# Kernel optimization log

Measured on AMD Instinct MI355X. Metric: run time of the kernel, lower is better.

## Reference

```python
import jax, jax.numpy as jnp
import numpy as np

B, S, H, NH = 8, 2048, 128, 4
HS = H // NH
EPS = 1e-8


def setup_inputs() -> dict:
    key = jax.random.key(0)
    ks = jax.random.split(key, 20)
    sc = 1.0 / np.sqrt(H)
    d = {
        'item_embeds': jax.random.normal(ks[0], (B, S, H), jnp.float32),
        'behavior_embeds': jax.random.normal(ks[1], (B, S, H), jnp.float32),
        'attn_mask': jnp.zeros((B, 1, S, S), jnp.float32),
    }
    names = ['Wq', 'Wk', 'Wv', 'Wqb', 'Wkb', 'Wvb', 'Wf']
    for i, n in enumerate(names):
        d[n] = jax.random.normal(ks[2 + i], (H, H), jnp.float32) * sc
        d['b' + n[1:]] = jnp.zeros((H,), jnp.float32)
    d['ln_w'] = jnp.ones((H,), jnp.float32)
    d['ln_b'] = jnp.zeros((H,), jnp.float32)
    return d


def _split_heads(x):
    # [B,S,H] -> [B,NH,S,HS]
    return x.reshape(B, S, NH, HS).transpose(0, 2, 1, 3)


def _layer_norm(x, w, b):
    u = jnp.mean(x, -1, keepdims=True)
    s = jnp.mean((x - u) ** 2, -1, keepdims=True)
    return w * ((x - u) / jnp.sqrt(s + EPS)) + b


def reference(item_embeds, behavior_embeds, attn_mask,
              Wq, bq, Wk, bk, Wv, bv,
              Wqb, bqb, Wkb, bkb, Wvb, bvb,
              Wf, bf, ln_w, ln_b):
    Q = _split_heads(item_embeds @ Wq + bq)
    K = _split_heads(item_embeds @ Wk + bk)
    V = _split_heads(item_embeds @ Wv + bv)
    Qb = _split_heads(behavior_embeds @ Wqb + bqb)
    Kb = _split_heads(behavior_embeds @ Wkb + bkb)
    # V_behavior computed in the original forward but unused downstream
    _Vb = _split_heads(behavior_embeds @ Wvb + bvb)
    scores = (jnp.einsum('bhqd,bhkd->bhqk', Q, K)
              + jnp.einsum('bhqd,bhkd->bhqk', Qb, Kb)) / np.sqrt(HS)
    scores = scores + attn_mask
    probs = jax.nn.softmax(scores, axis=-1)
    attn_out = jnp.einsum('bhqk,bhkd->bhqd', probs, V)
    attn_out = attn_out.transpose(0, 2, 1, 3).reshape(B, S, H)
    out = attn_out @ Wf + bf
    return _layer_norm(out + item_embeds, ln_w, ln_b)
```

## Files before the change

kernel.cpp:

```cpp
#include <hip/hip_runtime.h>
#include <math.h>

typedef unsigned short ushort_t;
typedef __attribute__((ext_vector_type(8))) short bf16x8;
typedef __attribute__((ext_vector_type(4))) float f32x4;

namespace {
constexpr int B = 8, S = 2048, H = 128, NH = 4, HS = 32;
constexpr float EPS = 1e-8f;
constexpr float SCALE = 0.17677669529663687f;
constexpr float LOG2E = 1.4426950408889634f;
constexpr float SCALEL = SCALE * LOG2E;
constexpr int QT = 16, KT = 64;
constexpr int KS = 2;
constexpr int SKT = S / KS / KT;
constexpr int NE = B * S * H;
}

__device__ __forceinline__ ushort_t f2bf(float f) {
  unsigned u = __float_as_uint(f);
  unsigned r = (u + 0x7FFFu + ((u >> 16) & 1u)) >> 16;
  return (ushort_t)r;
}

__device__ __forceinline__ f32x4 mfma16(bf16x8 a, bf16x8 b, f32x4 c) {
  return __builtin_amdgcn_mfma_f32_16x16x32_bf16(a, b, c, 0, 0, 0);
}

__global__ __launch_bounds__(256) void mflag_kernel(
    const float* __restrict__ mask, unsigned* __restrict__ fm)
{
  const int qt = blockIdx.x;
  const int b  = blockIdx.y;
  const int z  = blockIdx.z;
  const int t = threadIdx.x;
  const int lt = t >> 6;
  const int lane = t & 63;
  const float* mp = mask + ((long)b * S + (long)qt * QT + (lane >> 4) * 4) * S
                  + z * 256 + lt * 64 + (lane & 15) * 4;
  float s = 0.f;
#pragma unroll
  for (int rr = 0; rr < 4; ++rr) {
    const float4 a = *(const float4*)&mp[(long)rr * S];
    s += fabsf(a.x) + fabsf(a.y) + fabsf(a.z) + fabsf(a.w);
  }
  s += __shfl_xor(s, 1);
  s += __shfl_xor(s, 2);
  s += __shfl_xor(s, 4);
  s += __shfl_xor(s, 8);
  s += __shfl_xor(s, 16);
  s += __shfl_xor(s, 32);
  if (lane == 0 && !(s == 0.f))
    atomicOr(&fm[b * (S / QT) + qt], 1u << (z * 4 + lt));
}

__global__ __launch_bounds__(256) void wcvt_kernel(
    const float* __restrict__ Wq, const float* __restrict__ Wk, const float* __restrict__ Wv,
    const float* __restrict__ Wqb, const float* __restrict__ Wkb, const float* __restrict__ Wf,
    ushort_t* __restrict__ Wt)
{
  const float* Ws[6] = {Wq, Wk, Wv, Wqb, Wkb, Wf};
  const float scl[6] = {SCALEL, 1.f, 1.f, SCALEL, 1.f, 1.f};
  const int m = blockIdx.y;
  const int kb = blockIdx.x;
  const float* W = Ws[m];
  const float sc = scl[m];
  __shared__ float T[32 * 132];
  const int t = threadIdx.x;
#pragma unroll
  for (int u = 0; u < 4; ++u) {
    const int idx = u * 256 + t;
    const int row = idx >> 5, c4 = idx & 31;
    const float4 v = *(const float4*)&W[(kb * 32 + row) * H + c4 * 4];
    *(float4*)&T[row * 132 + c4 * 4] = v;
  }
  __syncthreads();
#pragma unroll
  for (int u = 0; u < 16; ++u) {
    const int idx = u * 256 + t;
    const int n = idx >> 5, kk = idx & 31;
    Wt[m * (H * H) + n * H + kb * 32 + kk] = f2bf(T[kk * 132 + n] * sc);
  }
}

__global__ __launch_bounds__(256) void proj_kernel(
    const float* __restrict__ item, const float* __restrict__ beh,
    const ushort_t* __restrict__ Wt,
    const float* __restrict__ bq, const float* __restrict__ bk, const float* __restrict__ bv,
    const float* __restrict__ bqb, const float* __restrict__ bkb,
    ushort_t* __restrict__ Qo, ushort_t* __restrict__ Ko, ushort_t* __restrict__ Qbo,
    ushort_t* __restrict__ Kbo, ushort_t* __restrict__ Vto)
{
  __shared__ ushort_t Xi[16 * 136];
  __shared__ ushort_t Xb[16 * 136];
  __shared__ ushort_t Yb[5][16 * 136];
  const int t = threadIdx.x;
  const long r0 = (long)blockIdx.x * 16;
#pragma unroll
  for (int u = 0; u < 2; ++u) {
    const int idx = u * 256 + t;
    const int row = idx >> 5, c4 = idx & 31;
    const float4 vi = *(const float4*)&item[(r0 + row) * H + c4 * 4];
    const float4 vb = *(const float4*)&beh[(r0 + row) * H + c4 * 4];
    unsigned long long pi = (unsigned long long)f2bf(vi.x) | ((unsigned long long)f2bf(vi.y) << 16)
        | ((unsigned long long)f2bf(vi.z) << 32) | ((unsigned long long)f2bf(vi.w) << 48);
    unsigned long long pb = (unsigned long long)f2bf(vb.x) | ((unsigned long long)f2bf(vb.y) << 16)
        | ((unsigned long long)f2bf(vb.z) << 32) | ((unsigned long long)f2bf(vb.w) << 48);
    *(unsigned long long*)&Xi[row * 136 + c4 * 4] = pi;
    *(unsigned long long*)&Xb[row * 136 + c4 * 4] = pb;
  }
  __syncthreads();

  const int w = t >> 6, l = t & 63, l15 = l & 15, quad = l >> 4;
  const int bb = (int)(r0 >> 11);
  const int s0 = (int)(r0 & (S - 1));
  const float* bias[5] = {bq, bk, bv, bqb, bkb};
  const float bscale[5] = {SCALEL, 1.f, 1.f, SCALEL, 1.f};

  bf16x8 afi[4], afb[4];
#pragma unroll
  for (int ks = 0; ks < 4; ++ks) {
    afi[ks] = *(const bf16x8*)&Xi[l15 * 136 + ks * 32 + quad * 8];
    afb[ks] = *(const bf16x8*)&Xb[l15 * 136 + ks * 32 + quad * 8];
  }

#pragma unroll
  for (int p = 0; p < 5; ++p) {
    f32x4 acc[2];
#pragma unroll
    for (int nt = 0; nt < 2; ++nt) {
      const float bcol = bias[p][w * 32 + nt * 16 + l15] * bscale[p];
      acc[nt] = (f32x4){bcol, bcol, bcol, bcol};
    }
    const ushort_t* Wp = Wt + p * (H * H);
    const bf16x8* af = (p < 3) ? afi : afb;
#pragma unroll
    for (int ks = 0; ks < 4; ++ks) {
      bf16x8 bfr[2];
#pragma unroll
      for (int nt = 0; nt < 2; ++nt)
        bfr[nt] = *(const bf16x8*)&Wp[(w * 32 + nt * 16 + l15) * H + ks * 32 + quad * 8];
#pragma unroll
      for (int nt = 0; nt < 2; ++nt)
        acc[nt] = mfma16(af[ks], bfr[nt], acc[nt]);
    }
#pragma unroll
    for (int nt = 0; nt < 2; ++nt)
#pragma unroll
      for (int r = 0; r < 4; ++r)
        Yb[p][(quad * 4 + r) * 136 + w * 32 + nt * 16 + l15] = f2bf(acc[nt][r]);
  }
  __syncthreads();
  {
    const int row = t >> 4, cb = (t & 15) * 8;
    const int h = cb >> 5, dd = cb & 31;
    const long gidx = ((long)(bb * NH + h) * S + s0 + row) * HS + dd;
    ushort_t* dsts4[4] = {Qo, Ko, Qbo, Kbo};
    const int psrc[4] = {0, 1, 3, 4};
#pragma unroll
    for (int i = 0; i < 4; ++i)
      *(uint4*)&dsts4[i][gidx] = *(const uint4*)&Yb[psrc[i]][row * 136 + cb];
    const int d = t >> 1, sh = (t & 1) * 8;
    const int nt = (s0 >> 4) & 3;
    const long vbase = ((long)(bb * NH + (d >> 5)) * HS + (d & 31)) * S + (s0 & ~63) + nt;
#pragma unroll
    for (int i = 0; i < 8; ++i)
      Vto[vbase + (long)(sh + i) * 4] = Yb[2][(sh + i) * 136 + d];
  }
}

__global__ __launch_bounds__(256, 4) void attn_kernel(
    const ushort_t* __restrict__ Q, const ushort_t* __restrict__ K,
    const ushort_t* __restrict__ Qb, const ushort_t* __restrict__ Kb,
    const ushort_t* __restrict__ Vt, const float* __restrict__ mask,
    const unsigned* __restrict__ fmg,
    ushort_t* __restrict__ PO, float* __restrict__ lsumP)
{
  __shared__ ushort_t Pb[NH][16 * 72];
  const int t = threadIdx.x;
  const int w = t >> 6;
  const int l15 = t & 15, quad = (t & 63) >> 4;
  const int q0 = blockIdx.x * QT;
  const int b = blockIdx.y;
  const int kz = blockIdx.z;
  const int kbase = kz * (S / KS);
  const long hQ = (long)(b * NH + w) * S * HS;
  const long hV = (long)(b * NH + w) * HS * S;

  const bf16x8 qf  = *(const bf16x8*)&Q[hQ + (long)(q0 + l15) * HS + quad * 8];
  const bf16x8 qbf = *(const bf16x8*)&Qb[hQ + (long)(q0 + l15) * HS + quad * 8];

  const unsigned fm = fmg[b * (S / QT) + blockIdx.x];

  const float* mrow[4];
#pragma unroll
  for (int r = 0; r < 4; ++r)
    mrow[r] = mask + ((long)b * S + q0 + quad * 4 + r) * S + l15;

  float lsum[4] = {0.f, 0.f, 0.f, 0.f};
  f32x4 O[2];
#pragma unroll
  for (int dt = 0; dt < 2; ++dt) O[dt] = (f32x4){0.f, 0.f, 0.f, 0.f};
  ushort_t* Pw = Pb[w];

  for (int i = 0; i < SKT; ++i) {
    const int k0 = kbase + i * KT;
    bf16x8 kf[4], kbf[4], vf[2][2];
#pragma unroll
    for (int nt = 0; nt < 4; ++nt) {
      kf[nt]  = *(const bf16x8*)&K[hQ + (long)(k0 + nt * 16 + l15) * HS + quad * 8];
      kbf[nt] = *(const bf16x8*)&Kb[hQ + (long)(k0 + nt * 16 + l15) * HS + quad * 8];
    }
#pragma unroll
    for (int dt = 0; dt < 2; ++dt)
#pragma unroll
      for (int ks = 0; ks < 2; ++ks)
        vf[dt][ks] = *(const bf16x8*)&Vt[hV + (long)(dt * 16 + l15) * S + k0 + ks * 32 + quad * 8];
    f32x4 sc[4];
    if ((fm >> (kz * SKT + i)) & 1u) {
#pragma unroll
      for (int nt = 0; nt < 4; ++nt)
#pragma unroll
        for (int r = 0; r < 4; ++r)
          sc[nt][r] = mrow[r][k0 + nt * 16] * LOG2E;
    } else {
#pragma unroll
      for (int nt = 0; nt < 4; ++nt)
        sc[nt] = (f32x4){0.f, 0.f, 0.f, 0.f};
    }
#pragma unroll
    for (int nt = 0; nt < 4; ++nt) {
      sc[nt] = mfma16(qbf, kbf[nt], sc[nt]);
      sc[nt] = mfma16(qf, kf[nt], sc[nt]);
    }
#pragma unroll
    for (int nt = 0; nt < 4; ++nt)
#pragma unroll
      for (int r = 0; r < 4; ++r)
        sc[nt][r] = __builtin_amdgcn_exp2f(sc[nt][r]);
#pragma unroll
    for (int r = 0; r < 4; ++r)
      lsum[r] += sc[0][r] + sc[1][r] + sc[2][r] + sc[3][r];
#pragma unroll
    for (int r = 0; r < 4; ++r) {
      const unsigned long long pk =
            (unsigned long long)(__float_as_uint(sc[0][r]) >> 16)
          | ((unsigned long long)(__float_as_uint(sc[1][r]) >> 16) << 16)
          | ((unsigned long long)(__float_as_uint(sc[2][r]) >> 16) << 32)
          | ((unsigned long long)(__float_as_uint(sc[3][r]) >> 16) << 48);
      *(unsigned long long*)&Pw[(quad * 4 + r) * 72 + l15 * 4] = pk;
    }
    bf16x8 pf[2];
#pragma unroll
    for (int ks = 0; ks < 2; ++ks)
      pf[ks] = *(const bf16x8*)&Pw[l15 * 72 + ks * 32 + quad * 8];
#pragma unroll
    for (int dt = 0; dt < 2; ++dt)
#pragma unroll
      for (int ks = 0; ks < 2; ++ks)
        O[dt] = mfma16(pf[ks], vf[dt][ks], O[dt]);
  }
#pragma unroll
  for (int r = 0; r < 4; ++r) {
    float s = lsum[r];
    s += __shfl_xor(s, 1);
    s += __shfl_xor(s, 2);
    s += __shfl_xor(s, 4);
    s += __shfl_xor(s, 8);
    lsum[r] = s;
  }
#pragma unroll
  for (int r = 0; r < 4; ++r) {
    const long row = (long)b * S + q0 + quad * 4 + r;
#pragma unroll
    for (int dt = 0; dt < 2; ++dt)
      PO[(long)kz * NE + row * H + w * 32 + dt * 16 + l15] = f2bf(O[dt][r]);
    if (l15 == 0)
      lsumP[((long)(kz * B + b) * NH + w) * S + q0 + quad * 4 + r] = lsum[r];
  }
}

__global__ __launch_bounds__(256) void out_kernel(
    const ushort_t* __restrict__ PO, const float* __restrict__ lsumP,
    const float* __restrict__ item,
    const ushort_t* __restrict__ Wft, const float* __restrict__ bf_,
    const float* __restrict__ lnw, const float* __restrict__ lnb,
    float* __restrict__ out)
{
  __shared__ ushort_t As[16 * 136];
  __shared__ float Ys[16 * 132];
  const int t = threadIdx.x;
  const long r0 = (long)blockIdx.x * 16;
  {
    const int row = t >> 4, c8 = t & 15;
    const long grow = r0 + row;
    const int b = (int)(grow >> 11);
    const int s = (int)(grow & (S - 1));
    const int h = c8 >> 2;
    const float l = lsumP[((long)(0 * B + b) * NH + h) * S + s]
                  + lsumP[((long)(1 * B + b) * NH + h) * S + s];
    const float inv = 1.f / l;
    const long gi = grow * H + c8 * 8;
    const uint4 a0 = *(const uint4*)&PO[gi];
    const uint4 a1 = *(const uint4*)&PO[(long)NE + gi];
    const unsigned av0[4] = {a0.x, a0.y, a0.z, a0.w};
    const unsigned av1[4] = {a1.x, a1.y, a1.z, a1.w};
    unsigned rv[4];
#pragma unroll
    for (int i = 0; i < 4; ++i) {
      const float lo = (__uint_as_float(av0[i] << 16) + __uint_as_float(av1[i] << 16)) * inv;
      const float hi = (__uint_as_float(av0[i] & 0xFFFF0000u)
                      + __uint_as_float(av1[i] & 0xFFFF0000u)) * inv;
      rv[i] = (unsigned)f2bf(lo) | ((unsigned)f2bf(hi) << 16);
    }
    uint4 res; res.x = rv[0]; res.y = rv[1]; res.z = rv[2]; res.w = rv[3];
    *(uint4*)&As[row * 136 + c8 * 8] = res;
  }
  __syncthreads();
  const int w = t >> 6, l15 = t & 15, quad = (t & 63) >> 4;
  f32x4 acc[2];
#pragma unroll
  for (int nt = 0; nt < 2; ++nt) {
    const float bcol = bf_[w * 32 + nt * 16 + l15];
    acc[nt] = (f32x4){bcol, bcol, bcol, bcol};
  }
#pragma unroll
  for (int ks = 0; ks < 4; ++ks) {
    const bf16x8 a = *(const bf16x8*)&As[l15 * 136 + ks * 32 + quad * 8];
#pragma unroll
    for (int nt = 0; nt < 2; ++nt) {
      const bf16x8 bfr = *(const bf16x8*)&Wft[(w * 32 + nt * 16 + l15) * H + ks * 32 + quad * 8];
      acc[nt] = mfma16(a, bfr, acc[nt]);
    }
  }
#pragma unroll
  for (int nt = 0; nt < 2; ++nt)
#pragma unroll
    for (int r = 0; r < 4; ++r) {
      const int rl = quad * 4 + r;
      const int col = w * 32 + nt * 16 + l15;
      Ys[rl * 132 + col] = acc[nt][r] + item[(r0 + rl) * H + col];
    }
  __syncthreads();
  const int rl = t >> 4, ch = t & 15;
  float v[8];
#pragma unroll
  for (int g = 0; g < 2; ++g) {
    const float4 y = *(const float4*)&Ys[rl * 132 + ch * 8 + g * 4];
    v[g * 4 + 0] = y.x; v[g * 4 + 1] = y.y; v[g * 4 + 2] = y.z; v[g * 4 + 3] = y.w;
  }
  float s = 0.f;
#pragma unroll
  for (int i = 0; i < 8; ++i) s += v[i];
  s += __shfl_xor(s, 1);
  s += __shfl_xor(s, 2);
  s += __shfl_xor(s, 4);
  s += __shfl_xor(s, 8);
  const float u_ = s * (1.f / H);
  float s2 = 0.f;
#pragma unroll
  for (int i = 0; i < 8; ++i) { const float d = v[i] - u_; s2 += d * d; }
  s2 += __shfl_xor(s2, 1);
  s2 += __shfl_xor(s2, 2);
  s2 += __shfl_xor(s2, 4);
  s2 += __shfl_xor(s2, 8);
  const float rinv = rsqrtf(s2 * (1.f / H) + EPS);
#pragma unroll
  for (int g = 0; g < 2; ++g) {
    float4 o;
    const int col = ch * 8 + g * 4;
    o.x = lnw[col + 0] * ((v[g * 4 + 0] - u_) * rinv) + lnb[col + 0];
    o.y = lnw[col + 1] * ((v[g * 4 + 1] - u_) * rinv) + lnb[col + 1];
    o.z = lnw[col + 2] * ((v[g * 4 + 2] - u_) * rinv) + lnb[col + 2];
    o.w = lnw[col + 3] * ((v[g * 4 + 3] - u_) * rinv) + lnb[col + 3];
    *(float4*)&out[(r0 + rl) * H + col] = o;
  }
}

extern "C" void kernel_launch(void* const* d_in, const int* in_sizes, int n_in,
                              void* d_out, int out_size, void* d_ws, size_t ws_size,
                              hipStream_t stream) {
  const float* item = (const float*)d_in[0];
  const float* beh  = (const float*)d_in[1];
  const float* mask = (const float*)d_in[2];
  const float* Wq  = (const float*)d_in[3];  const float* bq  = (const float*)d_in[4];
  const float* Wk  = (const float*)d_in[5];  const float* bk  = (const float*)d_in[6];
  const float* Wv  = (const float*)d_in[7];  const float* bv  = (const float*)d_in[8];
  const float* Wqb = (const float*)d_in[9];  const float* bqb = (const float*)d_in[10];
  const float* Wkb = (const float*)d_in[11]; const float* bkb = (const float*)d_in[12];
  const float* Wf  = (const float*)d_in[15]; const float* bfv = (const float*)d_in[16];
  const float* lnw = (const float*)d_in[17]; const float* lnb = (const float*)d_in[18];
  float* out = (float*)d_out;

  ushort_t* ws = (ushort_t*)d_ws;
  ushort_t* Qw   = ws;
  ushort_t* Kw   = Qw + NE;
  ushort_t* Qbw  = Kw + NE;
  ushort_t* Kbw  = Qbw + NE;
  ushort_t* Vtw  = Kbw + NE;
  ushort_t* PO   = Vtw + NE;
  ushort_t* Wt   = PO + (long)KS * NE;
  unsigned* fm   = (unsigned*)(Wt + 6 * H * H);
  float* lsumP   = (float*)(fm + B * (S / QT));

  hipMemsetAsync(fm, 0, B * (S / QT) * sizeof(unsigned), stream);
  mflag_kernel<<<dim3(S / QT, B, 8), 256, 0, stream>>>(mask, fm);
  wcvt_kernel<<<dim3(4, 6), 256, 0, stream>>>(Wq, Wk, Wv, Wqb, Wkb, Wf, Wt);
  proj_kernel<<<dim3((B * S) / 16), 256, 0, stream>>>(
      item, beh, Wt, bq, bk, bv, bqb, bkb, Qw, Kw, Qbw, Kbw, Vtw);
  attn_kernel<<<dim3(S / QT, B, KS), 256, 0, stream>>>(
      Qw, Kw, Qbw, Kbw, Vtw, mask, fm, PO, lsumP);
  out_kernel<<<dim3((B * S) / 16), 256, 0, stream>>>(
      PO, lsumP, item, Wt + 5 * H * H, bfv, lnw, lnb, out);
}
```

Before: 395.9 us.

## Double-buffer K tiles in attention and fold mask-flag memset into kernel

```diff
diff --git a/kernel.cpp b/kernel.cpp
--- a/kernel.cpp
+++ b/kernel.cpp
@@ -32,26 +32,26 @@
 {
   const int qt = blockIdx.x;
   const int b  = blockIdx.y;
-  const int z  = blockIdx.z;
   const int t = threadIdx.x;
-  const int lt = t >> 6;
-  const int lane = t & 63;
-  const float* mp = mask + ((long)b * S + (long)qt * QT + (lane >> 4) * 4) * S
-                  + z * 256 + lt * 64 + (lane & 15) * 4;
+  __shared__ unsigned fmask;
+  if (t == 0) fmask = 0u;
+  __syncthreads();
+  const float* mp = mask + ((long)b * S + (long)qt * QT) * S + t * 8;
   float s = 0.f;
-#pragma unroll
-  for (int rr = 0; rr < 4; ++rr) {
-    const float4 a = *(const float4*)&mp[(long)rr * S];
-    s += fabsf(a.x) + fabsf(a.y) + fabsf(a.z) + fabsf(a.w);
+#pragma unroll 4
+  for (int row = 0; row < QT; ++row) {
+    const float4 a = *(const float4*)&mp[(long)row * S];
+    const float4 c = *(const float4*)&mp[(long)row * S + 4];
+    s += fabsf(a.x) + fabsf(a.y) + fabsf(a.z) + fabsf(a.w)
+       + fabsf(c.x) + fabsf(c.y) + fabsf(c.z) + fabsf(c.w);
   }
   s += __shfl_xor(s, 1);
   s += __shfl_xor(s, 2);
   s += __shfl_xor(s, 4);
-  s += __shfl_xor(s, 8);
-  s += __shfl_xor(s, 16);
-  s += __shfl_xor(s, 32);
-  if (lane == 0 && !(s == 0.f))
-    atomicOr(&fm[b * (S / QT) + qt], 1u << (z * 4 + lt));
+  if ((t & 7) == 0 && !(s == 0.f))
+    atomicOr(&fmask, 1u << (t >> 3));
+  __syncthreads();
+  if (t == 0) fm[b * (S / QT) + qt] = fmask;
 }
 
 __global__ __launch_bounds__(256) void wcvt_kernel(
@@ -169,7 +169,74 @@
   }
 }
 
-__global__ __launch_bounds__(256, 4) void attn_kernel(
+__device__ __forceinline__ void attn_step(
+    int k0, int kn, bool msknz,
+    const bf16x8 (&kfc)[4], const bf16x8 (&kbfc)[4],
+    bf16x8 (&kfn)[4], bf16x8 (&kbfn)[4],
+    const bf16x8& qf, const bf16x8& qbf,
+    const ushort_t* __restrict__ K, const ushort_t* __restrict__ Kb,
+    const ushort_t* __restrict__ Vt,
+    long hQ, long hV, const float* const (&mrow)[4],
+    int l15, int quad, ushort_t* Pw,
+    float (&lsum)[4], f32x4 (&O)[2])
+{
+  bf16x8 vf[2][2];
+#pragma unroll
+  for (int dt = 0; dt < 2; ++dt)
+#pragma unroll
+    for (int ks = 0; ks < 2; ++ks)
+      vf[dt][ks] = *(const bf16x8*)&Vt[hV + (long)(dt * 16 + l15) * S + k0 + ks * 32 + quad * 8];
+#pragma unroll
+  for (int nt = 0; nt < 4; ++nt) {
+    kfn[nt]  = *(const bf16x8*)&K[hQ + (long)(kn + nt * 16 + l15) * HS + quad * 8];
+    kbfn[nt] = *(const bf16x8*)&Kb[hQ + (long)(kn + nt * 16 + l15) * HS + quad * 8];
+  }
+  f32x4 sc[4];
+  if (msknz) {
+#pragma unroll
+    for (int nt = 0; nt < 4; ++nt)
+#pragma unroll
+      for (int r = 0; r < 4; ++r)
+        sc[nt][r] = mrow[r][k0 + nt * 16] * LOG2E;
+  } else {
+#pragma unroll
+    for (int nt = 0; nt < 4; ++nt)
+      sc[nt] = (f32x4){0.f, 0.f, 0.f, 0.f};
+  }
+#pragma unroll
+  for (int nt = 0; nt < 4; ++nt) {
+    sc[nt] = mfma16(qbf, kbfc[nt], sc[nt]);
+    sc[nt] = mfma16(qf, kfc[nt], sc[nt]);
+  }
+#pragma unroll
+  for (int nt = 0; nt < 4; ++nt)
+#pragma unroll
+    for (int r = 0; r < 4; ++r)
+      sc[nt][r] = __builtin_amdgcn_exp2f(sc[nt][r]);
+#pragma unroll
+  for (int r = 0; r < 4; ++r)
+    lsum[r] += sc[0][r] + sc[1][r] + sc[2][r] + sc[3][r];
+#pragma unroll
+  for (int r = 0; r < 4; ++r) {
+    const unsigned long long pk =
+          (unsigned long long)(__float_as_uint(sc[0][r]) >> 16)
+        | ((unsigned long long)(__float_as_uint(sc[1][r]) >> 16) << 16)
+        | ((unsigned long long)(__float_as_uint(sc[2][r]) >> 16) << 32)
+        | ((unsigned long long)(__float_as_uint(sc[3][r]) >> 16) << 48);
+    *(unsigned long long*)&Pw[(quad * 4 + r) * 72 + l15 * 4] = pk;
+  }
+  bf16x8 pf[2];
+#pragma unroll
+  for (int ks = 0; ks < 2; ++ks)
+    pf[ks] = *(const bf16x8*)&Pw[l15 * 72 + ks * 32 + quad * 8];
+#pragma unroll
+  for (int dt = 0; dt < 2; ++dt)
+#pragma unroll
+    for (int ks = 0; ks < 2; ++ks)
+      O[dt] = mfma16(pf[ks], vf[dt][ks], O[dt]);
+}
+
+__global__ __launch_bounds__(256, 2) void attn_kernel(
     const ushort_t* __restrict__ Q, const ushort_t* __restrict__ K,
     const ushort_t* __restrict__ Qb, const ushort_t* __restrict__ Kb,
     const ushort_t* __restrict__ Vt, const float* __restrict__ mask,
@@ -203,62 +270,21 @@
   for (int dt = 0; dt < 2; ++dt) O[dt] = (f32x4){0.f, 0.f, 0.f, 0.f};
   ushort_t* Pw = Pb[w];
 
-  for (int i = 0; i < SKT; ++i) {
+  bf16x8 kfA[4], kbfA[4], kfB[4], kbfB[4];
+#pragma unroll
+  for (int nt = 0; nt < 4; ++nt) {
+    kfA[nt]  = *(const bf16x8*)&K[hQ + (long)(kbase + nt * 16 + l15) * HS + quad * 8];
+    kbfA[nt] = *(const bf16x8*)&Kb[hQ + (long)(kbase + nt * 16 + l15) * HS + quad * 8];
+  }
+
+  for (int i = 0; i < SKT; i += 2) {
     const int k0 = kbase + i * KT;
-    bf16x8 kf[4], kbf[4], vf[2][2];
-#pragma unroll
-    for (int nt = 0; nt < 4; ++nt) {
-      kf[nt]  = *(const bf16x8*)&K[hQ + (long)(k0 + nt * 16 + l15) * HS + quad * 8];
-      kbf[nt] = *(const bf16x8*)&Kb[hQ + (long)(k0 + nt * 16 + l15) * HS + quad * 8];
-    }
-#pragma unroll
-    for (int dt = 0; dt < 2; ++dt)
-#pragma unroll
-      for (int ks = 0; ks < 2; ++ks)
-        vf[dt][ks] = *(const bf16x8*)&Vt[hV + (long)(dt * 16 + l15) * S + k0 + ks * 32 + quad * 8];
-    f32x4 sc[4];
-    if ((fm >> (kz * SKT + i)) & 1u) {
-#pragma unroll
-      for (int nt = 0; nt < 4; ++nt)
-#pragma unroll
-        for (int r = 0; r < 4; ++r)
-          sc[nt][r] = mrow[r][k0 + nt * 16] * LOG2E;
-    } else {
-#pragma unroll
-      for (int nt = 0; nt < 4; ++nt)
-        sc[nt] = (f32x4){0.f, 0.f, 0.f, 0.f};
-    }
-#pragma unroll
-    for (int nt = 0; nt < 4; ++nt) {
-      sc[nt] = mfma16(qbf, kbf[nt], sc[nt]);
-      sc[nt] = mfma16(qf, kf[nt], sc[nt]);
-    }
-#pragma unroll
-    for (int nt = 0; nt < 4; ++nt)
-#pragma unroll
-      for (int r = 0; r < 4; ++r)
-        sc[nt][r] = __builtin_amdgcn_exp2f(sc[nt][r]);
-#pragma unroll
-    for (int r = 0; r < 4; ++r)
-      lsum[r] += sc[0][r] + sc[1][r] + sc[2][r] + sc[3][r];
-#pragma unroll
-    for (int r = 0; r < 4; ++r) {
-      const unsigned long long pk =
-            (unsigned long long)(__float_as_uint(sc[0][r]) >> 16)
-          | ((unsigned long long)(__float_as_uint(sc[1][r]) >> 16) << 16)
-          | ((unsigned long long)(__float_as_uint(sc[2][r]) >> 16) << 32)
-          | ((unsigned long long)(__float_as_uint(sc[3][r]) >> 16) << 48);
-      *(unsigned long long*)&Pw[(quad * 4 + r) * 72 + l15 * 4] = pk;
-    }
-    bf16x8 pf[2];
-#pragma unroll
-    for (int ks = 0; ks < 2; ++ks)
-      pf[ks] = *(const bf16x8*)&Pw[l15 * 72 + ks * 32 + quad * 8];
-#pragma unroll
-    for (int dt = 0; dt < 2; ++dt)
-#pragma unroll
-      for (int ks = 0; ks < 2; ++ks)
-        O[dt] = mfma16(pf[ks], vf[dt][ks], O[dt]);
+    const int kn1 = k0 + KT;
+    const int kn2 = (i + 2 < SKT) ? k0 + 2 * KT : kbase;
+    attn_step(k0, kn1, (fm >> (kz * SKT + i)) & 1u, kfA, kbfA, kfB, kbfB,
+              qf, qbf, K, Kb, Vt, hQ, hV, mrow, l15, quad, Pw, lsum, O);
+    attn_step(kn1, kn2, (fm >> (kz * SKT + i + 1)) & 1u, kfB, kbfB, kfA, kbfA,
+              qf, qbf, K, Kb, Vt, hQ, hV, mrow, l15, quad, Pw, lsum, O);
   }
 #pragma unroll
   for (int r = 0; r < 4; ++r) {
@@ -403,8 +429,7 @@
   unsigned* fm   = (unsigned*)(Wt + 6 * H * H);
   float* lsumP   = (float*)(fm + B * (S / QT));
 
-  hipMemsetAsync(fm, 0, B * (S / QT) * sizeof(unsigned), stream);
-  mflag_kernel<<<dim3(S / QT, B, 8), 256, 0, stream>>>(mask, fm);
+  mflag_kernel<<<dim3(S / QT, B), 256, 0, stream>>>(mask, fm);
   wcvt_kernel<<<dim3(4, 6), 256, 0, stream>>>(Wq, Wk, Wv, Wqb, Wkb, Wf, Wt);
   proj_kernel<<<dim3((B * S) / 16), 256, 0, stream>>>(
       item, beh, Wt, bq, bk, bv, bqb, bkb, Qw, Kw, Qbw, Kbw, Vtw);
```

Result: no change. 400.3 us (+1.1%).
